# Optimization experiments

Hardware: AMD Instinct MI355X
Metric: run time of the kernel (lower is better)

Reference implementation:

```python
import jax, jax.numpy as jnp
import numpy as np

B, N, D_MODEL, H = 2, 2048, 1024, 16
Q_CHUNK, K_CHUNK = 512, 1024
LN_EPS = 1e-5


def layer_norm(x, g, b):
    mu = x.mean(-1, keepdims=True)
    var = ((x - mu) ** 2).mean(-1, keepdims=True)
    return (x - mu) * jax.lax.rsqrt(var + LN_EPS) * g + b


def chunked_attention(q, k, v, qry_chunk, key_chunk):
    # q,k,v: [b,h,n,d]; memory-efficient chunked online-softmax attention
    b, h, n, d = q.shape
    q = q * (d ** -0.5)
    Q, K = n // qry_chunk, n // key_chunk
    qr = q.reshape(b, h, Q, qry_chunk, d)
    kr = k.reshape(b, h, K, key_chunk, d)
    vr = v.reshape(b, h, K, key_chunk, d)
    # per (q-chunk, k-chunk) scores: [b,h,Q,K,i,j]
    qk = jnp.einsum('bhqid,bhkjd->bhqkij', qr, kr)
    qk_max = jax.lax.stop_gradient(qk.max(axis=-1, keepdims=True))  # [b,h,Q,K,i,1]
    exp_qk = jnp.exp(qk - qk_max)
    attn = jnp.einsum('bhqkij,bhkjd->bhqkid', exp_qk, vr)
    exp_sum = exp_qk.sum(-1)            # [b,h,Q,K,i]
    m = qk_max[..., 0]                  # [b,h,Q,K,i]
    gmax = m.max(axis=3, keepdims=True)  # global max over key chunks
    renorm = jax.lax.stop_gradient(jnp.exp(m - gmax))
    num = (attn * renorm[..., None]).sum(axis=3)       # [b,h,Q,i,d]
    den = (exp_sum * renorm).sum(axis=3)[..., None]    # [b,h,Q,i,1]
    out = num / (1e-8 + den)
    return out.reshape(b, h, n, d)


def setup_inputs() -> dict:
    key = jax.random.key(0)
    ks = jax.random.split(key, 10)
    s = 0.02
    return {
        'x': jax.random.normal(ks[0], (B, N, D_MODEL), dtype=jnp.float32),
        'Wq': jax.random.normal(ks[1], (D_MODEL, D_MODEL), dtype=jnp.float32) * s,
        'bq': jnp.zeros((D_MODEL,), jnp.float32),
        'Wk': jax.random.normal(ks[2], (D_MODEL, D_MODEL), dtype=jnp.float32) * s,
        'bk': jnp.zeros((D_MODEL,), jnp.float32),
        'Wv': jax.random.normal(ks[3], (D_MODEL, D_MODEL), dtype=jnp.float32) * s,
        'bv': jnp.zeros((D_MODEL,), jnp.float32),
        'Wo': jax.random.normal(ks[4], (D_MODEL, D_MODEL), dtype=jnp.float32) * s,
        'bo': jnp.zeros((D_MODEL,), jnp.float32),
        'ln_g': jnp.ones((D_MODEL,), jnp.float32),
        'ln_b': jnp.zeros((D_MODEL,), jnp.float32),
    }


def reference(x, Wq, bq, Wk, bk, Wv, bv, Wo, bo, ln_g, ln_b):
    # qkv adapter: self-attention (key = val = qry = x)
    q = x @ Wq + bq
    k = x @ Wk + bk
    v = x @ Wv + bv
    # pre-norm on query path
    q = layer_norm(q, ln_g, ln_b)
    b, n, _ = q.shape
    d = D_MODEL // H
    qh = q.reshape(b, n, H, d).transpose(0, 2, 1, 3)
    kh = k.reshape(b, n, H, d).transpose(0, 2, 1, 3)
    vh = v.reshape(b, n, H, d).transpose(0, 2, 1, 3)
    attn = chunked_attention(qh, kh, vh, Q_CHUNK, K_CHUNK)
    out = attn.transpose(0, 2, 1, 3).reshape(b, n, D_MODEL)
    out = out + q  # residual with normed projected query
    return out @ Wo + bo
```

## Files before the change

### kernel.cpp

```cpp
#include <hip/hip_runtime.h>


typedef unsigned short u16;
typedef __attribute__((ext_vector_type(8))) short bf8v;
typedef __attribute__((ext_vector_type(4))) float f4v;

typedef __attribute__((address_space(1))) void gvoid;
typedef __attribute__((address_space(3))) void lvoid;
__device__ __forceinline__ void cp16(const void* g, void* l) {
  __builtin_amdgcn_global_load_lds((gvoid*)g, (lvoid*)l, 16, 0, 0);
}

__device__ __forceinline__ float bf2f(u16 u) {
  unsigned int x = ((unsigned int)u) << 16;
  float f; __builtin_memcpy(&f, &x, 4); return f;
}
__device__ __forceinline__ u16 f2bf(float f) {
  unsigned int x; __builtin_memcpy(&x, &f, 4);
  unsigned int r = (x + 0x7fffu + ((x >> 16) & 1u)) >> 16;
  return (u16)r;
}
__device__ __forceinline__ unsigned pack2bf(float a, float b) {
  unsigned ua, ub;
  __builtin_memcpy(&ua, &a, 4); __builtin_memcpy(&ub, &b, 4);
  return __builtin_amdgcn_perm(ub, ua, 0x07060302u);
}

#define KSCALE 0.18033688011f

__global__ __launch_bounds__(256) void k_preprocess(
    const u16* a0, const u16* a1, const u16* a2, const u16* a3,
    const u16* a4, const u16* a5, const u16* a6, const u16* a7,
    const u16* a8, const u16* a9, const u16* a10,
    u16* xb, u16* wt, int* flags) {
  const int blk = blockIdx.x;
  const int t = threadIdx.x;
  __shared__ u16 tile[64 * 65];
  __shared__ int cls[3];

  if (blk >= 3072) {
    if (t >= 11) return;
    const u16* arr[11] = {a0,a1,a2,a3,a4,a5,a6,a7,a8,a9,a10};
    const u16* p = arr[t];
    int ze = 0, no = 0, pe = 0;
    for (int i = 0; i < 128; ++i) {
      u16 he = p[2*i], ho = p[2*i+1];
      if (he == 0) ze++;
      if (ho != 0) no++;
      int e = (he >> 7) & 0xff;
      if (he == 0 || (e >= 64 && e <= 160)) pe++;
    }
    int isbf;
    if (ze >= 100 && no >= 64) isbf = 0;
    else isbf = (pe >= 100) ? 1 : 0;
    flags[t] = isbf;
    return;
  }

  int wz = (blk - 2048) >> 8;
  const u16* src = (blk < 2048) ? a0
                 : (wz == 0) ? a1 : (wz == 1) ? a3 : (wz == 2) ? a5 : a7;
  if (t == 0) { cls[0] = 0; cls[1] = 0; cls[2] = 0; }
  __syncthreads();
  if (t < 128) {
    u16 he = src[2*t], ho = src[2*t+1];
    int e = (he >> 7) & 0xff;
    if (he == 0) atomicAdd(&cls[0], 1);
    if (ho != 0) atomicAdd(&cls[1], 1);
    if (he == 0 || (e >= 64 && e <= 160)) atomicAdd(&cls[2], 1);
  }
  __syncthreads();
  int isbf;
  if (cls[0] >= 100 && cls[1] >= 64) isbf = 0;
  else isbf = (cls[2] >= 100) ? 1 : 0;

  if (blk < 2048) {
    size_t i = ((size_t)blk * 256 + t) * 8;
    if (isbf) {
      *(float4*)(xb + i) = *((const float4*)(a0 + i));
    } else {
      const float* xf = (const float*)a0;
      float4 a = *(const float4*)(xf + i);
      float4 b = *(const float4*)(xf + i + 4);
      ushort4 o0, o1;
      o0.x = f2bf(a.x); o0.y = f2bf(a.y); o0.z = f2bf(a.z); o0.w = f2bf(a.w);
      o1.x = f2bf(b.x); o1.y = f2bf(b.y); o1.z = f2bf(b.z); o1.w = f2bf(b.w);
      *(ushort4*)(xb + i) = o0; *(ushort4*)(xb + i + 4) = o1;
    }
    return;
  }

  {
    int rem = (blk - 2048) & 255;
    int r0 = ((rem >> 4) & 15) * 64, c0 = (rem & 15) * 64;
    u16* dst = wt + (size_t)wz * (1u << 20);
    for (int rr = 0; rr < 2; ++rr) {
      int row = rr * 32 + (t >> 3);
      int c8 = (t & 7) * 8;
      u16 v[8];
      if (isbf) {
        const u16* Ws = src;
        ushort4 a = *(const ushort4*)&Ws[(size_t)(r0 + row) * 1024 + c0 + c8];
        ushort4 b = *(const ushort4*)&Ws[(size_t)(r0 + row) * 1024 + c0 + c8 + 4];
        v[0]=a.x; v[1]=a.y; v[2]=a.z; v[3]=a.w; v[4]=b.x; v[5]=b.y; v[6]=b.z; v[7]=b.w;
      } else {
        const float* Wf = (const float*)src;
        float4 a = *(const float4*)&Wf[(size_t)(r0 + row) * 1024 + c0 + c8];
        float4 b = *(const float4*)&Wf[(size_t)(r0 + row) * 1024 + c0 + c8 + 4];
        v[0]=f2bf(a.x); v[1]=f2bf(a.y); v[2]=f2bf(a.z); v[3]=f2bf(a.w);
        v[4]=f2bf(b.x); v[5]=f2bf(b.y); v[6]=f2bf(b.z); v[7]=f2bf(b.w);
      }
#pragma unroll
      for (int j = 0; j < 8; ++j) tile[row * 65 + c8 + j] = v[j];
    }
    __syncthreads();
    for (int rr = 0; rr < 2; ++rr) {
      int nrow = rr * 32 + (t >> 3);
      int k8 = (t & 7) * 8;
      u16 v[8];
#pragma unroll
      for (int j = 0; j < 8; ++j) v[j] = tile[(k8 + j) * 65 + nrow];
      ushort4 o0, o1;
      o0.x=v[0]; o0.y=v[1]; o0.z=v[2]; o0.w=v[3];
      o1.x=v[4]; o1.y=v[5]; o1.z=v[6]; o1.w=v[7];
      *(ushort4*)&dst[(size_t)(c0 + nrow) * 1024 + r0 + k8] = o0;
      *(ushort4*)&dst[(size_t)(c0 + nrow) * 1024 + r0 + k8 + 4] = o1;
    }
  }
}

template <int MT>
__device__ __forceinline__ void gemm_bt(const u16* __restrict__ A, const u16* __restrict__ Bt,
    const void* __restrict__ bias, int bias_bf, void* __restrict__ Cout, int mode,
    float cscale) {
  constexpr int MI = MT / 32;
  __shared__ __align__(16) u16 As[2][MT * 32];
  __shared__ __align__(16) u16 Bs[2][128 * 32];
  const int tid = threadIdx.x;
  const int wave = tid >> 6, lane = tid & 63;
  const int qd = lane >> 4, ln = lane & 15;
  const int m0 = blockIdx.y * MT, n0 = blockIdx.x * 128;
  const int wr = (wave >> 1) * (MT / 2), wc = (wave & 1) * 64;
  const int r0 = wave * 16 + (lane >> 2);
  const int csrc = ((lane & 3) ^ ((lane >> 2) & 3)) * 8;
  const u16* Ag = &A[(size_t)m0 * 1024];
  const u16* Bg = &Bt[(size_t)n0 * 1024];
  const int co = (qd ^ (ln & 3)) * 8;
  f4v acc[MI][4];
#pragma unroll
  for (int i = 0; i < MI; ++i)
#pragma unroll
    for (int j = 0; j < 4; ++j) acc[i][j] = (f4v){0.f, 0.f, 0.f, 0.f};

#pragma unroll
  for (int t = 0; t < MT / 64; ++t)
    cp16(&Ag[(size_t)(t * 64 + r0) * 1024 + csrc], &As[0][(t * 256 + wave * 64) * 8]);
#pragma unroll
  for (int t = 0; t < 2; ++t)
    cp16(&Bg[(size_t)(t * 64 + r0) * 1024 + csrc], &Bs[0][(t * 256 + wave * 64) * 8]);

  for (int it = 0; it < 32; ++it) {
    __syncthreads();
    if (it < 31) {
      int ko = (it + 1) * 32;
      int bi = (it + 1) & 1;
#pragma unroll
      for (int t = 0; t < MT / 64; ++t)
        cp16(&Ag[(size_t)(t * 64 + r0) * 1024 + ko + csrc], &As[bi][(t * 256 + wave * 64) * 8]);
#pragma unroll
      for (int t = 0; t < 2; ++t)
        cp16(&Bg[(size_t)(t * 64 + r0) * 1024 + ko + csrc], &Bs[bi][(t * 256 + wave * 64) * 8]);
    }
    const u16* as = As[it & 1];
    const u16* bs = Bs[it & 1];
    bf8v af[MI], bfr[4];
#pragma unroll
    for (int i = 0; i < MI; ++i) af[i]  = *(const bf8v*)&as[(wr + i * 16 + ln) * 32 + co];
#pragma unroll
    for (int j = 0; j < 4; ++j) bfr[j] = *(const bf8v*)&bs[(wc + j * 16 + ln) * 32 + co];
#pragma unroll
    for (int i = 0; i < MI; ++i)
#pragma unroll
      for (int j = 0; j < 4; ++j)
        acc[i][j] = __builtin_amdgcn_mfma_f32_16x16x32_bf16(af[i], bfr[j], acc[i][j], 0, 0, 0);
  }
#pragma unroll
  for (int j = 0; j < 4; ++j) {
    int col = n0 + wc + j * 16 + ln;
    float bv = bias_bf ? bf2f(((const u16*)bias)[col]) : ((const float*)bias)[col];
#pragma unroll
    for (int i = 0; i < MI; ++i) {
      int row = m0 + wr + i * 16 + qd * 4;
      if (mode == 2) {
        ushort4 o4;
        o4.x = f2bf((acc[i][j][0] + bv) * cscale);
        o4.y = f2bf((acc[i][j][1] + bv) * cscale);
        o4.z = f2bf((acc[i][j][2] + bv) * cscale);
        o4.w = f2bf((acc[i][j][3] + bv) * cscale);
        int b_ = row >> 11, nl = row & 2047;
        int h_ = col >> 6, d6 = col & 63;
        int kt = nl >> 6, b0 = nl & 63;
        int c = b0 >> 5, g = (b0 >> 4) & 1, qd_f = (b0 >> 2) & 3;
        int dt = d6 >> 4, ln_f = d6 & 15;
        size_t off = (size_t)(b_ * 16 + h_) * 131072
                   + (size_t)(kt * 4096 + (c * 4 + dt) * 512 + (qd_f * 16 + ln_f) * 8 + g * 4);
        *(ushort4*)&((u16*)Cout)[off] = o4;
      } else if (mode == 3) {
        int b_ = row >> 11, nl = row & 2047;
        int h_ = col >> 6, d6 = col & 63;
        int tile = nl >> 6, ct = (nl >> 4) & 3;
        int half = d6 >> 5, qd_k = (d6 >> 3) & 3, jj = d6 & 7;
        size_t base = (size_t)(b_ * 16 + h_) * 131072
                    + (size_t)(tile * 4096 + (ct * 2 + half) * 512 + qd_k * 128 + jj);
#pragma unroll
        for (int r = 0; r < 4; ++r) {
          float v = (acc[i][j][r] + bv) * cscale;
          ((u16*)Cout)[base + (size_t)(((nl & 15) + r) * 8)] = f2bf(v);
        }
      } else {
#pragma unroll
        for (int r = 0; r < 4; ++r) {
          float v = (acc[i][j][r] + bv) * cscale;
          if (mode == 1) ((u16*)Cout)[(size_t)(row + r) * 1024 + col] = f2bf(v);
          else           ((float*)Cout)[(size_t)(row + r) * 1024 + col] = v;
        }
      }
    }
  }
}

__global__ __launch_bounds__(256) void k_gemm_qkv(const u16* xb, const u16* wt,
    const void* bq, const void* bk, const void* bv, const int* flags,
    u16* qpre, u16* kb, u16* vtb) {
  int z = blockIdx.z;
  const u16* Bt = wt + (size_t)z * (1u << 20);
  const void* bias = (z == 0) ? bq : (z == 1) ? bk : bv;
  if (z == 0)      gemm_bt<128>(xb, Bt, bias, flags[2], qpre, 1, 1.0f);
  else if (z == 1) gemm_bt<128>(xb, Bt, bias, flags[4], kb,   3, KSCALE);
  else             gemm_bt<128>(xb, Bt, bias, flags[6], vtb,  2, 1.0f);
}

__global__ __launch_bounds__(256) void k_gemm_out(const u16* A, const u16* Bt,
    const void* bias, const int* flags, void* out) {
  gemm_bt<64>(A, Bt, bias, flags[8], out, flags[0] ? 1 : 0, 1.0f);
}

__global__ __launch_bounds__(256) void k_layernorm(const u16* __restrict__ qp,
    const void* __restrict__ g, const void* __restrict__ bb, const int* flags,
    u16* __restrict__ out) {
  int row = blockIdx.x, t = threadIdx.x;
  const u16* rp = qp + (size_t)row * 1024;
  ushort4 u = *(const ushort4*)(rp + t * 4);
  float x0 = bf2f(u.x), x1 = bf2f(u.y), x2 = bf2f(u.z), x3 = bf2f(u.w);
  float s = x0 + x1 + x2 + x3;
  float s2 = x0 * x0 + x1 * x1 + x2 * x2 + x3 * x3;
  for (int off = 32; off; off >>= 1) { s += __shfl_down(s, off); s2 += __shfl_down(s2, off); }
  __shared__ float red[10];
  int wave = t >> 6, lane = t & 63;
  if (lane == 0) { red[wave] = s; red[4 + wave] = s2; }
  __syncthreads();
  if (t == 0) {
    float S = red[0] + red[1] + red[2] + red[3];
    float S2 = red[4] + red[5] + red[6] + red[7];
    float mu = S * (1.f / 1024.f);
    float var = S2 * (1.f / 1024.f) - mu * mu;
    red[8] = mu; red[9] = rsqrtf(var + 1e-5f);
  }
  __syncthreads();
  float mu = red[8], rstd = red[9];
  int gf = flags[9], bf = flags[10];
  int c = t * 4;
  float gv[4], bv[4];
#pragma unroll
  for (int k = 0; k < 4; ++k) {
    gv[k] = gf ? bf2f(((const u16*)g)[c + k]) : ((const float*)g)[c + k];
    bv[k] = bf ? bf2f(((const u16*)bb)[c + k]) : ((const float*)bb)[c + k];
  }
  ushort4 o;
  o.x = f2bf((x0 - mu) * rstd * gv[0] + bv[0]);
  o.y = f2bf((x1 - mu) * rstd * gv[1] + bv[1]);
  o.z = f2bf((x2 - mu) * rstd * gv[2] + bv[2]);
  o.w = f2bf((x3 - mu) * rstd * gv[3] + bv[3]);
  *(ushort4*)(out + (size_t)row * 1024 + c) = o;
}

template <int NQS>
__device__ __forceinline__ void attn_tile(const bf8v kf[4][2], const bf8v vf[8],
    const bf8v qf[NQS][2], float ls[NQS][4], f4v o[NQS][4]) {
#pragma unroll
  for (int qs = 0; qs < NQS; ++qs) {
    unsigned pk[4][2];
#pragma unroll
    for (int ct = 0; ct < 4; ++ct) {
      f4v z = (f4v){0.f, 0.f, 0.f, 0.f};
      z = __builtin_amdgcn_mfma_f32_16x16x32_bf16(kf[ct][0], qf[qs][0], z, 0, 0, 0);
      z = __builtin_amdgcn_mfma_f32_16x16x32_bf16(kf[ct][1], qf[qs][1], z, 0, 0, 0);
      float p0 = __builtin_amdgcn_exp2f(z[0]);
      float p1 = __builtin_amdgcn_exp2f(z[1]);
      float p2 = __builtin_amdgcn_exp2f(z[2]);
      float p3 = __builtin_amdgcn_exp2f(z[3]);
      ls[qs][0] += p0; ls[qs][1] += p1; ls[qs][2] += p2; ls[qs][3] += p3;
      pk[ct][0] = pack2bf(p0, p1);
      pk[ct][1] = pack2bf(p2, p3);
    }
#pragma unroll
    for (int c = 0; c < 2; ++c) {
      unsigned avals[4] = {pk[2*c][0], pk[2*c][1], pk[2*c+1][0], pk[2*c+1][1]};
      bf8v af; __builtin_memcpy(&af, avals, 16);
#pragma unroll
      for (int dt = 0; dt < 4; ++dt)
        o[qs][dt] = __builtin_amdgcn_mfma_f32_16x16x32_bf16(af, vf[c * 4 + dt], o[qs][dt], 0, 0, 0);
    }
  }
}

__global__ __launch_bounds__(256) void k_attention(const u16* __restrict__ qln,
    const u16* __restrict__ kfg, const u16* __restrict__ vfg, u16* __restrict__ attn) {
  const int x = blockIdx.x;
  const int xcd = x & 7, sl = x >> 3;
  const int bh = xcd * 4 + (sl >> 4), qc = sl & 15;
  const int b = bh >> 4, h = bh & 15;
  const int tid = threadIdx.x, wave = tid >> 6, lane = tid & 63;
  const int qd = lane >> 4, ln = lane & 15;
  const int qrow0 = qc * 128 + wave * 32;

  const u16* kgb = kfg + (size_t)bh * 131072;
  const u16* vgb = vfg + (size_t)bh * 131072;

  __shared__ __align__(16) u16 kv[2][8192];

  bf8v qf[2][2];
#pragma unroll
  for (int qs = 0; qs < 2; ++qs) {
    const u16* qb = qln + ((size_t)b * 2048 + qrow0 + qs * 16 + ln) * 1024 + h * 64;
    qf[qs][0] = *(const bf8v*)(qb + qd * 8);
    qf[qs][1] = *(const bf8v*)(qb + 32 + qd * 8);
  }
  float ls[2][4];
  f4v o[2][4];
#pragma unroll
  for (int qs = 0; qs < 2; ++qs)
#pragma unroll
    for (int r = 0; r < 4; ++r) { ls[qs][r] = 0.f; o[qs][r] = (f4v){0.f, 0.f, 0.f, 0.f}; }

#pragma unroll
  for (int q = 0; q < 2; ++q) {
    cp16(kgb + (size_t)(q * 256 + tid) * 8, &kv[0][(q * 256 + wave * 64) * 8]);
    cp16(vgb + (size_t)(q * 256 + tid) * 8, &kv[0][4096 + (q * 256 + wave * 64) * 8]);
  }

  for (int t = 0; t < 32; ++t) {
    __syncthreads();
    if (t < 31) {
      const u16* ks = kgb + (size_t)(t + 1) * 4096;
      const u16* vs = vgb + (size_t)(t + 1) * 4096;
      u16* dst = kv[(t + 1) & 1];
#pragma unroll
      for (int q = 0; q < 2; ++q) {
        cp16(ks + (size_t)(q * 256 + tid) * 8, &dst[(q * 256 + wave * 64) * 8]);
        cp16(vs + (size_t)(q * 256 + tid) * 8, &dst[4096 + (q * 256 + wave * 64) * 8]);
      }
    }
    const u16* kvb = kv[t & 1];
    bf8v kfr[4][2], vfr[8];
#pragma unroll
    for (int ct = 0; ct < 4; ++ct) {
      kfr[ct][0] = *(const bf8v*)&kvb[(ct * 2 + 0) * 512 + lane * 8];
      kfr[ct][1] = *(const bf8v*)&kvb[(ct * 2 + 1) * 512 + lane * 8];
    }
#pragma unroll
    for (int cd = 0; cd < 8; ++cd)
      vfr[cd] = *(const bf8v*)&kvb[4096 + cd * 512 + lane * 8];
    attn_tile<2>(kfr, vfr, qf, ls, o);
  }

#pragma unroll
  for (int qs = 0; qs < 2; ++qs) {
    float lsum = (ls[qs][0] + ls[qs][1]) + (ls[qs][2] + ls[qs][3]);
    lsum += __shfl_xor(lsum, 16);
    lsum += __shfl_xor(lsum, 32);
    float rden[4];
#pragma unroll
    for (int r = 0; r < 4; ++r) {
      float dv = __shfl(lsum, (lane & 48) + qd * 4 + r);
      rden[r] = __builtin_amdgcn_rcpf(1e-8f + dv);
    }
#pragma unroll
    for (int dt = 0; dt < 4; ++dt) {
#pragma unroll
      for (int r = 0; r < 4; ++r) {
        size_t idx = ((size_t)b * 2048 + qrow0 + qs * 16 + qd * 4 + r) * 1024
                   + h * 64 + dt * 16 + ln;
        float val = o[qs][dt][r] * rden[r] + bf2f(qln[idx]);
        attn[idx] = f2bf(val);
      }
    }
  }
}

extern "C" void kernel_launch(void* const* d_in, const int* in_sizes, int n_in,
                              void* d_out, int out_size, void* d_ws, size_t ws_size,
                              hipStream_t stream) {
  int* flags = (int*)d_ws;
  u16* base = (u16*)((char*)d_ws + 256);
  const size_t M1 = 1u << 20;
  u16* xb   = base;
  u16* wt   = base + 4 * M1;
  u16* qpre = base + 8 * M1;
  u16* kb   = base + 12 * M1;
  u16* vtb  = base + 16 * M1;
  u16* qln = xb;
  u16* at  = qpre;

  k_preprocess<<<3073, 256, 0, stream>>>(
      (const u16*)d_in[0], (const u16*)d_in[1], (const u16*)d_in[2], (const u16*)d_in[3],
      (const u16*)d_in[4], (const u16*)d_in[5], (const u16*)d_in[6], (const u16*)d_in[7],
      (const u16*)d_in[8], (const u16*)d_in[9], (const u16*)d_in[10], xb, wt, flags);
  k_gemm_qkv<<<dim3(8, 32, 3), 256, 0, stream>>>(xb, wt, d_in[2], d_in[4], d_in[6], flags,
                                                 qpre, kb, vtb);
  k_layernorm<<<4096, 256, 0, stream>>>(qpre, d_in[9], d_in[10], flags, qln);
  k_attention<<<512, 256, 0, stream>>>(qln, kb, vtb, at);
  k_gemm_out<<<dim3(8, 64), 256, 0, stream>>>(at, wt + 3 * M1, d_in[8], flags, d_out);
}
```

Baseline: 214.2 us.

## Fuse query layernorm into QKV GEMM epilogue and attention prologue

Removes the standalone layernorm kernel. The Q-projection GEMM epilogue now accumulates per-row sum and sum-of-squares into a float stats buffer with atomics, and the preprocess kernel zeroes that buffer first. The attention kernel then normalizes the query fragments on load and recomputes the normalized query for the residual add from the raw projection. This cuts one launch and a full read/write pass over the query tensor. In exchange it adds atomic traffic, a variance computed as E[x²]−mu² in the epilogue, and redundant gamma/beta loads in attention.

```diff
diff --git a/kernel.cpp b/kernel.cpp
--- a/kernel.cpp
+++ b/kernel.cpp
@@ -32,13 +32,19 @@
     const u16* a0, const u16* a1, const u16* a2, const u16* a3,
     const u16* a4, const u16* a5, const u16* a6, const u16* a7,
     const u16* a8, const u16* a9, const u16* a10,
-    u16* xb, u16* wt, int* flags) {
+    u16* xb, u16* wt, int* flags, float* stats) {
   const int blk = blockIdx.x;
   const int t = threadIdx.x;
   __shared__ u16 tile[64 * 65];
   __shared__ int cls[3];
 
   if (blk >= 3072) {
+    if (blk < 3076) {
+      size_t i = ((size_t)(blk - 3072) * 256 + t) * 8;
+      *(float4*)(stats + i) = (float4){0.f, 0.f, 0.f, 0.f};
+      *(float4*)(stats + i + 4) = (float4){0.f, 0.f, 0.f, 0.f};
+      return;
+    }
     if (t >= 11) return;
     const u16* arr[11] = {a0,a1,a2,a3,a4,a5,a6,a7,a8,a9,a10};
     const u16* p = arr[t];
@@ -132,7 +138,7 @@
 template <int MT>
 __device__ __forceinline__ void gemm_bt(const u16* __restrict__ A, const u16* __restrict__ Bt,
     const void* __restrict__ bias, int bias_bf, void* __restrict__ Cout, int mode,
-    float cscale) {
+    float cscale, float* __restrict__ stats = nullptr) {
   constexpr int MI = MT / 32;
   __shared__ __align__(16) u16 As[2][MT * 32];
   __shared__ __align__(16) u16 Bs[2][128 * 32];
@@ -221,8 +227,38 @@
 #pragma unroll
         for (int r = 0; r < 4; ++r) {
           float v = (acc[i][j][r] + bv) * cscale;
-          if (mode == 1) ((u16*)Cout)[(size_t)(row + r) * 1024 + col] = f2bf(v);
-          else           ((float*)Cout)[(size_t)(row + r) * 1024 + col] = v;
+          if (mode == 0) ((float*)Cout)[(size_t)(row + r) * 1024 + col] = v;
+          else           ((u16*)Cout)[(size_t)(row + r) * 1024 + col] = f2bf(v);
+        }
+      }
+    }
+  }
+  if (mode == 4) {
+    float bvs[4];
+#pragma unroll
+    for (int j = 0; j < 4; ++j) {
+      int col = n0 + wc + j * 16 + ln;
+      bvs[j] = bias_bf ? bf2f(((const u16*)bias)[col]) : ((const float*)bias)[col];
+    }
+#pragma unroll
+    for (int i = 0; i < MI; ++i) {
+#pragma unroll
+      for (int r = 0; r < 4; ++r) {
+        float pv = 0.f, pv2 = 0.f;
+#pragma unroll
+        for (int j = 0; j < 4; ++j) {
+          float v = (acc[i][j][r] + bvs[j]) * cscale;
+          float vr = bf2f(f2bf(v));
+          pv += vr; pv2 += vr * vr;
+        }
+        pv += __shfl_xor(pv, 1);  pv2 += __shfl_xor(pv2, 1);
+        pv += __shfl_xor(pv, 2);  pv2 += __shfl_xor(pv2, 2);
+        pv += __shfl_xor(pv, 4);  pv2 += __shfl_xor(pv2, 4);
+        pv += __shfl_xor(pv, 8);  pv2 += __shfl_xor(pv2, 8);
+        if (ln == 0) {
+          int row = m0 + wr + i * 16 + qd * 4 + r;
+          atomicAdd(&stats[2 * row], pv);
+          atomicAdd(&stats[2 * row + 1], pv2);
         }
       }
     }
@@ -231,11 +267,11 @@
 
 __global__ __launch_bounds__(256) void k_gemm_qkv(const u16* xb, const u16* wt,
     const void* bq, const void* bk, const void* bv, const int* flags,
-    u16* qpre, u16* kb, u16* vtb) {
+    u16* qpre, u16* kb, u16* vtb, float* stats) {
   int z = blockIdx.z;
   const u16* Bt = wt + (size_t)z * (1u << 20);
   const void* bias = (z == 0) ? bq : (z == 1) ? bk : bv;
-  if (z == 0)      gemm_bt<128>(xb, Bt, bias, flags[2], qpre, 1, 1.0f);
+  if (z == 0)      gemm_bt<128>(xb, Bt, bias, flags[2], qpre, 4, 1.0f, stats);
   else if (z == 1) gemm_bt<128>(xb, Bt, bias, flags[4], kb,   3, KSCALE);
   else             gemm_bt<128>(xb, Bt, bias, flags[6], vtb,  2, 1.0f);
 }
@@ -243,45 +279,6 @@
 __global__ __launch_bounds__(256) void k_gemm_out(const u16* A, const u16* Bt,
     const void* bias, const int* flags, void* out) {
   gemm_bt<64>(A, Bt, bias, flags[8], out, flags[0] ? 1 : 0, 1.0f);
-}
-
-__global__ __launch_bounds__(256) void k_layernorm(const u16* __restrict__ qp,
-    const void* __restrict__ g, const void* __restrict__ bb, const int* flags,
-    u16* __restrict__ out) {
-  int row = blockIdx.x, t = threadIdx.x;
-  const u16* rp = qp + (size_t)row * 1024;
-  ushort4 u = *(const ushort4*)(rp + t * 4);
-  float x0 = bf2f(u.x), x1 = bf2f(u.y), x2 = bf2f(u.z), x3 = bf2f(u.w);
-  float s = x0 + x1 + x2 + x3;
-  float s2 = x0 * x0 + x1 * x1 + x2 * x2 + x3 * x3;
-  for (int off = 32; off; off >>= 1) { s += __shfl_down(s, off); s2 += __shfl_down(s2, off); }
-  __shared__ float red[10];
-  int wave = t >> 6, lane = t & 63;
-  if (lane == 0) { red[wave] = s; red[4 + wave] = s2; }
-  __syncthreads();
-  if (t == 0) {
-    float S = red[0] + red[1] + red[2] + red[3];
-    float S2 = red[4] + red[5] + red[6] + red[7];
-    float mu = S * (1.f / 1024.f);
-    float var = S2 * (1.f / 1024.f) - mu * mu;
-    red[8] = mu; red[9] = rsqrtf(var + 1e-5f);
-  }
-  __syncthreads();
-  float mu = red[8], rstd = red[9];
-  int gf = flags[9], bf = flags[10];
-  int c = t * 4;
-  float gv[4], bv[4];
-#pragma unroll
-  for (int k = 0; k < 4; ++k) {
-    gv[k] = gf ? bf2f(((const u16*)g)[c + k]) : ((const float*)g)[c + k];
-    bv[k] = bf ? bf2f(((const u16*)bb)[c + k]) : ((const float*)bb)[c + k];
-  }
-  ushort4 o;
-  o.x = f2bf((x0 - mu) * rstd * gv[0] + bv[0]);
-  o.y = f2bf((x1 - mu) * rstd * gv[1] + bv[1]);
-  o.z = f2bf((x2 - mu) * rstd * gv[2] + bv[2]);
-  o.w = f2bf((x3 - mu) * rstd * gv[3] + bv[3]);
-  *(ushort4*)(out + (size_t)row * 1024 + c) = o;
 }
 
 template <int NQS>
@@ -314,8 +311,11 @@
   }
 }
 
-__global__ __launch_bounds__(256) void k_attention(const u16* __restrict__ qln,
-    const u16* __restrict__ kfg, const u16* __restrict__ vfg, u16* __restrict__ attn) {
+__global__ __launch_bounds__(256) void k_attention(const u16* __restrict__ qpre,
+    const u16* __restrict__ kfg, const u16* __restrict__ vfg,
+    const float* __restrict__ stats, const void* __restrict__ gg,
+    const void* __restrict__ bbv, const int* __restrict__ flags,
+    u16* __restrict__ attn) {
   const int x = blockIdx.x;
   const int xcd = x & 7, sl = x >> 3;
   const int bh = xcd * 4 + (sl >> 4), qc = sl & 15;
@@ -326,15 +326,35 @@
 
   const u16* kgb = kfg + (size_t)bh * 131072;
   const u16* vgb = vfg + (size_t)bh * 131072;
+  const int gf = flags[9], bfl = flags[10];
 
   __shared__ __align__(16) u16 kv[2][8192];
 
   bf8v qf[2][2];
 #pragma unroll
   for (int qs = 0; qs < 2; ++qs) {
-    const u16* qb = qln + ((size_t)b * 2048 + qrow0 + qs * 16 + ln) * 1024 + h * 64;
-    qf[qs][0] = *(const bf8v*)(qb + qd * 8);
-    qf[qs][1] = *(const bf8v*)(qb + 32 + qd * 8);
+    int rowg = b * 2048 + qrow0 + qs * 16 + ln;
+    float s = stats[2 * rowg], s2 = stats[2 * rowg + 1];
+    float mu = s * (1.f / 1024.f);
+    float rs = rsqrtf(s2 * (1.f / 1024.f) - mu * mu + 1e-5f);
+    const u16* qb = qpre + (size_t)rowg * 1024 + h * 64;
+#pragma unroll
+    for (int half = 0; half < 2; ++half) {
+      bf8v raw = *(const bf8v*)(qb + half * 32 + qd * 8);
+      unsigned pkq[4];
+#pragma unroll
+      for (int e = 0; e < 4; ++e) {
+        int c0 = h * 64 + half * 32 + qd * 8 + 2 * e;
+        float g0 = gf ? bf2f(((const u16*)gg)[c0])     : ((const float*)gg)[c0];
+        float g1 = gf ? bf2f(((const u16*)gg)[c0 + 1]) : ((const float*)gg)[c0 + 1];
+        float b0 = bfl ? bf2f(((const u16*)bbv)[c0])     : ((const float*)bbv)[c0];
+        float b1 = bfl ? bf2f(((const u16*)bbv)[c0 + 1]) : ((const float*)bbv)[c0 + 1];
+        float v0 = bf2f((u16)raw[2 * e]);
+        float v1 = bf2f((u16)raw[2 * e + 1]);
+        pkq[e] = pack2bf((v0 - mu) * rs * g0 + b0, (v1 - mu) * rs * g1 + b1);
+      }
+      __builtin_memcpy(&qf[qs][half], pkq, 16);
+    }
   }
   float ls[2][4];
   f4v o[2][4];
@@ -379,19 +399,26 @@
     float lsum = (ls[qs][0] + ls[qs][1]) + (ls[qs][2] + ls[qs][3]);
     lsum += __shfl_xor(lsum, 16);
     lsum += __shfl_xor(lsum, 32);
-    float rden[4];
+    float rden[4], mur[4], rsr[4];
 #pragma unroll
     for (int r = 0; r < 4; ++r) {
       float dv = __shfl(lsum, (lane & 48) + qd * 4 + r);
       rden[r] = __builtin_amdgcn_rcpf(1e-8f + dv);
+      int rowg = b * 2048 + qrow0 + qs * 16 + qd * 4 + r;
+      float s = stats[2 * rowg], s2 = stats[2 * rowg + 1];
+      mur[r] = s * (1.f / 1024.f);
+      rsr[r] = rsqrtf(s2 * (1.f / 1024.f) - mur[r] * mur[r] + 1e-5f);
     }
 #pragma unroll
     for (int dt = 0; dt < 4; ++dt) {
+      int c = h * 64 + dt * 16 + ln;
+      float gvv = gf ? bf2f(((const u16*)gg)[c]) : ((const float*)gg)[c];
+      float bvv = bfl ? bf2f(((const u16*)bbv)[c]) : ((const float*)bbv)[c];
 #pragma unroll
       for (int r = 0; r < 4; ++r) {
-        size_t idx = ((size_t)b * 2048 + qrow0 + qs * 16 + qd * 4 + r) * 1024
-                   + h * 64 + dt * 16 + ln;
-        float val = o[qs][dt][r] * rden[r] + bf2f(qln[idx]);
+        size_t idx = ((size_t)b * 2048 + qrow0 + qs * 16 + qd * 4 + r) * 1024 + c;
+        float qv = bf2f(qpre[idx]);
+        float val = o[qs][dt][r] * rden[r] + (qv - mur[r]) * rsr[r] * gvv + bvv;
         attn[idx] = f2bf(val);
       }
     }
@@ -409,16 +436,15 @@
   u16* qpre = base + 8 * M1;
   u16* kb   = base + 12 * M1;
   u16* vtb  = base + 16 * M1;
-  u16* qln = xb;
+  float* stats = (float*)(base + 20 * M1);
   u16* at  = qpre;
 
-  k_preprocess<<<3073, 256, 0, stream>>>(
+  k_preprocess<<<3077, 256, 0, stream>>>(
       (const u16*)d_in[0], (const u16*)d_in[1], (const u16*)d_in[2], (const u16*)d_in[3],
       (const u16*)d_in[4], (const u16*)d_in[5], (const u16*)d_in[6], (const u16*)d_in[7],
-      (const u16*)d_in[8], (const u16*)d_in[9], (const u16*)d_in[10], xb, wt, flags);
+      (const u16*)d_in[8], (const u16*)d_in[9], (const u16*)d_in[10], xb, wt, flags, stats);
   k_gemm_qkv<<<dim3(8, 32, 3), 256, 0, stream>>>(xb, wt, d_in[2], d_in[4], d_in[6], flags,
-                                                 qpre, kb, vtb);
-  k_layernorm<<<4096, 256, 0, stream>>>(qpre, d_in[9], d_in[10], flags, qln);
-  k_attention<<<512, 256, 0, stream>>>(qln, kb, vtb, at);
+                                                 qpre, kb, vtb, stats);
+  k_attention<<<512, 256, 0, stream>>>(qpre, kb, vtb, stats, d_in[9], d_in[10], flags, at);
   k_gemm_out<<<dim3(8, 64), 256, 0, stream>>>(at, wt + 3 * M1, d_in[8], flags, d_out);
 }
```

Result: slower. 225.0 us (+5.0%).
